# Optimization experiments

Hardware: AMD Instinct MI355X
Metric: run time of the kernel (lower is better)

Reference implementation:

```python
import jax, jax.numpy as jnp
import numpy as np

N = 100000
E = 3200000
NFEAT = 256
NHID = 256
NCLASS = 40


def _uniform(key, shape, stdv):
    return jax.random.uniform(key, shape, jnp.float32, -stdv, stdv)


def setup_inputs() -> dict:
    key = jax.random.key(0)
    ks = jax.random.split(key, 16)
    x = jax.random.normal(ks[0], (N, NFEAT), jnp.float32)
    edge_row = jax.random.randint(ks[1], (E,), 0, N, jnp.int32)
    edge_col = jax.random.randint(ks[2], (E,), 0, N, jnp.int32)
    edge_weight = jax.random.uniform(ks[3], (E,), jnp.float32)
    # MyLinear init: stdv = 1/sqrt(out_features)
    dims = [(NFEAT, NHID), (NHID, NHID), (NHID, NHID), (NHID, NCLASS)]
    params = {}
    for i, (fi, fo) in enumerate(dims):
        stdv = 1.0 / np.sqrt(fo)
        params[f"W{i+1}"] = _uniform(ks[4 + 2 * i], (fi, fo), stdv)
        params[f"b{i+1}"] = _uniform(ks[5 + 2 * i], (fo,), stdv)
    return dict(x=x, edge_row=edge_row, edge_col=edge_col, edge_weight=edge_weight, **params)


def _spmm(edge_row, edge_col, edge_weight, x):
    # out[i] = sum_{(i,j) in E} w_ij * x[j]
    msgs = edge_weight[:, None] * x[edge_col]  # [E, d]
    return jax.ops.segment_sum(msgs, edge_row, num_segments=N)


def reference(x, edge_row, edge_col, edge_weight, W1, b1, W2, b2, W3, b3, W4, b4):
    # layer 0 (ix % mlp_layers == 0 -> residual + spmm)
    h = x + _spmm(edge_row, edge_col, edge_weight, x)
    h = jax.nn.relu(h @ W1 + b1)
    # layer 1
    h = jax.nn.relu(h @ W2 + b2)
    # layer 2 (spmm + residual again)
    h = h + _spmm(edge_row, edge_col, edge_weight, h)
    h = jax.nn.relu(h @ W3 + b3)
    # layer 3 (final, no relu)
    h = h @ W4 + b4
    return jax.nn.log_softmax(h, axis=1)
```

## Files before the change

kernel.cpp:

```cpp
#include <hip/hip_runtime.h>
#include <hip/hip_bf16.h>
#include <cstdint>

#define N_NODES 100000
#define N_EDGES 3200000
#define NFEAT   256
#define NCLASS  40

#define BROWS_LOG 7
#define BROWS     128
#define NBUCK     782
#define CHUNK     8192
#define NBLK      391
#define GHN       (NBUCK * NBLK)

typedef __bf16 bf16;
typedef __attribute__((ext_vector_type(8))) __bf16 bf16x8;
typedef __attribute__((ext_vector_type(4))) float f32x4;
typedef __attribute__((ext_vector_type(2))) float f32x2;

__device__ inline float b2f(unsigned short u) {
    union { unsigned int i; float f; } x; x.i = ((unsigned int)u) << 16; return x.f;
}
__device__ inline unsigned short f2b(float f) {
    union { float f; unsigned int i; } x; x.f = f;
    unsigned int i = x.i;
    return (unsigned short)((i + 0x7fffu + ((i >> 16) & 1u)) >> 16);
}
__device__ inline f32x2 unpack2(unsigned int d) {
    union { unsigned int i; float f; } lo, hi;
    lo.i = d << 16;
    hi.i = d & 0xFFFF0000u;
    return (f32x2){lo.f, hi.f};
}
__device__ inline unsigned int pack2(f32x2 a) {
    return ((unsigned int)f2b(a[0])) | (((unsigned int)f2b(a[1])) << 16);
}

__host__ __device__ inline int permN(int s) {
    return (((s >> 5) & 7) << 5) | (((s >> 2) & 3) << 3) | (((s >> 4) & 1) << 2) | (s & 3);
}

__global__ void prep_w_kernel(const float* __restrict__ W1, const float* __restrict__ W2,
                              const float* __restrict__ W3, const float* __restrict__ W4,
                              const float* __restrict__ b1, const float* __restrict__ b3,
                              unsigned short* __restrict__ WT1, unsigned short* __restrict__ WT2,
                              unsigned short* __restrict__ WT3, unsigned short* __restrict__ WT4,
                              float* __restrict__ b1p, float* __restrict__ b3p) {
    int i = blockIdx.x * blockDim.x + threadIdx.x;
    if (i < 256 * 256) {
        int s = i >> 8, k = i & 255;
        int n = permN(s);
        WT1[i] = f2b(W1[k * 256 + n]);
        WT2[i] = f2b(W2[k * 256 + s]);
        WT3[i] = f2b(W3[k * 256 + n]);
        if (k == 0) { b1p[s] = b1[n]; b3p[s] = b3[n]; }
    }
    if (i < 48 * 256) {
        int nIdx = i >> 8, k = i & 255;
        WT4[i] = (nIdx < NCLASS) ? f2b(W4[k * NCLASS + nIdx]) : (unsigned short)0;
    }
}

__global__ void cast_kernel(const float* __restrict__ X, unsigned short* __restrict__ Y, int n4) {
    int i = blockIdx.x * blockDim.x + threadIdx.x;
    if (i >= n4) return;
    float4 v = *(const float4*)(X + (size_t)i * 4);
    ushort4 o;
    o.x = f2b(v.x); o.y = f2b(v.y); o.z = f2b(v.z); o.w = f2b(v.w);
    *(ushort4*)(Y + (size_t)i * 4) = o;
}

__global__ __launch_bounds__(256) void p1a_kernel(const int* __restrict__ erow,
                                                  int* __restrict__ ghist) {
    __shared__ int h[NBUCK];
    for (int j = threadIdx.x; j < NBUCK; j += 256) h[j] = 0;
    __syncthreads();
    int base = blockIdx.x * CHUNK;
    for (int j = 0; j < CHUNK; j += 256) {
        int i = base + j + threadIdx.x;
        if (i < N_EDGES) atomicAdd(&h[erow[i] >> BROWS_LOG], 1);
    }
    __syncthreads();
    for (int j = threadIdx.x; j < NBUCK; j += 256)
        ghist[(size_t)j * NBLK + blockIdx.x] = h[j];
}

__global__ void scanB_blocks_kernel(int* __restrict__ g, int* __restrict__ bsums, int n) {
    __shared__ int s[1024];
    int i = blockIdx.x * 1024 + threadIdx.x;
    int v = (i < n) ? g[i] : 0;
    s[threadIdx.x] = v;
    __syncthreads();
    for (int off = 1; off < 1024; off <<= 1) {
        int t = (threadIdx.x >= off) ? s[threadIdx.x - off] : 0;
        __syncthreads();
        s[threadIdx.x] += t;
        __syncthreads();
    }
    if (i < n) g[i] = s[threadIdx.x] - v;
    if (threadIdx.x == 1023) bsums[blockIdx.x] = s[1023];
}

__global__ void scanB_sums_kernel(int* __restrict__ bsums, int nb) {
    __shared__ int s[512];
    int v = (threadIdx.x < nb) ? bsums[threadIdx.x] : 0;
    s[threadIdx.x] = v;
    __syncthreads();
    for (int off = 1; off < 512; off <<= 1) {
        int t = (threadIdx.x >= off) ? s[threadIdx.x - off] : 0;
        __syncthreads();
        s[threadIdx.x] += t;
        __syncthreads();
    }
    if (threadIdx.x < nb) bsums[threadIdx.x] = s[threadIdx.x] - v;
}

__global__ void scanB_add_kernel(int* __restrict__ g, const int* __restrict__ bsums, int n) {
    int i = blockIdx.x * blockDim.x + threadIdx.x;
    if (i < n) g[i] += bsums[i >> 10];
}

__global__ __launch_bounds__(256) void p1c_kernel(const int* __restrict__ erow,
                                                  const int* __restrict__ ecol,
                                                  const float* __restrict__ ew,
                                                  const int* __restrict__ ghist,
                                                  uint2* __restrict__ stage) {
    __shared__ int cur[NBUCK];
    for (int j = threadIdx.x; j < NBUCK; j += 256)
        cur[j] = ghist[(size_t)j * NBLK + blockIdx.x];
    __syncthreads();
    int base = blockIdx.x * CHUNK;
    for (int j = 0; j < CHUNK; j += 1024) {
        int r[4], c[4]; float w[4]; bool m[4];
#pragma unroll
        for (int q = 0; q < 4; q++) {
            int i = base + j + q * 256 + threadIdx.x;
            m[q] = (i < N_EDGES);
            if (m[q]) { r[q] = erow[i]; c[q] = ecol[i]; w[q] = ew[i]; }
        }
#pragma unroll
        for (int q = 0; q < 4; q++) {
            if (m[q]) {
                unsigned int qq = (unsigned int)(w[q] * 32768.f + 0.5f);
                if (qq > 32767u) qq = 32767u;
                int p = atomicAdd(&cur[r[q] >> BROWS_LOG], 1);
                stage[p] = make_uint2((unsigned int)r[q], (((unsigned int)c[q]) << 15) | qq);
            }
        }
    }
}

__global__ __launch_bounds__(256) void p2_kernel(const int* __restrict__ ghist,
                                                 const uint2* __restrict__ stage,
                                                 unsigned int* __restrict__ edges,
                                                 int* __restrict__ rowptr) {
    __shared__ int h[BROWS], sc[BROWS], lcur[BROWS];
    int b = blockIdx.x;
    int lo = ghist[(size_t)b * NBLK];
    int hi = (b + 1 < NBUCK) ? ghist[(size_t)(b + 1) * NBLK] : N_EDGES;
    if (threadIdx.x < BROWS) h[threadIdx.x] = 0;
    __syncthreads();
    for (int i = lo + threadIdx.x; i < hi; i += 256)
        atomicAdd(&h[stage[i].x & (BROWS - 1)], 1);
    __syncthreads();
    if (threadIdx.x < BROWS) sc[threadIdx.x] = h[threadIdx.x];
    __syncthreads();
    for (int off = 1; off < BROWS; off <<= 1) {
        int t = 0;
        if (threadIdx.x < BROWS && threadIdx.x >= off) t = sc[threadIdx.x - off];
        __syncthreads();
        if (threadIdx.x < BROWS) sc[threadIdx.x] += t;
        __syncthreads();
    }
    if (threadIdx.x < BROWS) {
        int ex = sc[threadIdx.x] - h[threadIdx.x];
        int row = b * BROWS + threadIdx.x;
        if (row <= N_NODES) rowptr[row] = lo + ex;
        lcur[threadIdx.x] = lo + ex;
    }
    __syncthreads();
    for (int i = lo + threadIdx.x; i < hi; i += 256) {
        uint2 sd = stage[i];
        int p = atomicAdd(&lcur[sd.x & (BROWS - 1)], 1);
        edges[p] = sd.y;
    }
}

__global__ void spmm_res_kernel(const unsigned short* __restrict__ X, unsigned short* __restrict__ Y,
                                const int* __restrict__ rowptr, const unsigned int* __restrict__ edges,
                                int n) {
    int gtid = blockIdx.x * blockDim.x + threadIdx.x;
    int row = gtid >> 6;
    int lane = gtid & 63;
    if (row >= n) return;
    const int half = lane >> 5;
    const int fb = (lane & 31) * 8;

    f32x2 acc[4];
    {
        uint4 xb = *(const uint4*)(X + (size_t)row * NFEAT + fb);
        if (half == 0) {
            acc[0] = unpack2(xb.x); acc[1] = unpack2(xb.y);
            acc[2] = unpack2(xb.z); acc[3] = unpack2(xb.w);
        } else {
            acc[0] = (f32x2){0.f, 0.f}; acc[1] = (f32x2){0.f, 0.f};
            acc[2] = (f32x2){0.f, 0.f}; acc[3] = (f32x2){0.f, 0.f};
        }
    }

    int s = rowptr[row], e = rowptr[row + 1];
    for (int k = s; k < e; k += 12) {
        int   c[6];
        f32x2 w2[6];
#pragma unroll
        for (int j = 0; j < 6; j++) {
            int kj = k + j * 2 + half;
            int kc = (kj < e) ? kj : (e - 1);
            unsigned int d = edges[kc];
            c[j] = (int)(d >> 15);
            float w = (kj < e) ? (float)(d & 32767u) * (1.f / 32768.f) : 0.f;
            w2[j] = (f32x2){w, w};
        }
        uint4 v[6];
#pragma unroll
        for (int j = 0; j < 6; j++) v[j] = *(const uint4*)(X + (size_t)c[j] * NFEAT + fb);
#pragma unroll
        for (int j = 0; j < 6; j++) {
            acc[0] += w2[j] * unpack2(v[j].x);
            acc[1] += w2[j] * unpack2(v[j].y);
            acc[2] += w2[j] * unpack2(v[j].z);
            acc[3] += w2[j] * unpack2(v[j].w);
        }
    }

#pragma unroll
    for (int i = 0; i < 4; i++) {
        acc[i][0] += __shfl_xor(acc[i][0], 32, 64);
        acc[i][1] += __shfl_xor(acc[i][1], 32, 64);
    }
    if (half == 0) {
        uint4 o;
        o.x = pack2(acc[0]); o.y = pack2(acc[1]);
        o.z = pack2(acc[2]); o.w = pack2(acc[3]);
        *(uint4*)(Y + (size_t)row * NFEAT + fb) = o;
    }
}

__global__ __launch_bounds__(256, 4) void gemm12_kernel(
    const bf16* __restrict__ X,
    const bf16* __restrict__ WT1p, const float* __restrict__ b1p,
    const bf16* __restrict__ WT2, const float* __restrict__ b2,
    unsigned short* __restrict__ Y, int M) {
    __shared__ unsigned int sB[256 * 20];
    const int tid = threadIdx.x;
    const int wave = tid >> 6;
    const int lane = tid & 63;
    const int m = lane & 15;
    const int quad = lane >> 4;
    const int lrow = wave * 16 + m;
    const int rowBase = blockIdx.x * 64;
    int arow = rowBase + lrow;
    if (arow >= M) arow = M - 1;

    f32x4 acc[16];
#pragma unroll
    for (int t = 0; t < 16; t++) acc[t] = (f32x4){0.f, 0.f, 0.f, 0.f};

    const bf16* xp = X + (size_t)arow * NFEAT + quad * 8;
#pragma unroll
    for (int k0 = 0; k0 < NFEAT; k0 += 32) {
#pragma unroll
        for (int f = tid; f < 1024; f += 256) {
            int n = f >> 2, j = f & 3;
            uint4 v = *(const uint4*)((const unsigned short*)WT1p + (size_t)n * NFEAT + k0 + j * 8);
            *(uint4*)&sB[n * 20 + j * 4] = v;
        }
        __syncthreads();
        bf16x8 a = *(const bf16x8*)(xp + k0);
#pragma unroll
        for (int t = 0; t < 16; t++) {
            bf16x8 b = *(const bf16x8*)&sB[(t * 16 + m) * 20 + quad * 4];
            acc[t] = __builtin_amdgcn_mfma_f32_16x16x32_bf16(b, a, acc[t], 0, 0, 0);
        }
        __syncthreads();
    }

    bf16x8 af[8];
#pragma unroll
    for (int kc = 0; kc < 8; kc++) {
        const float* p0 = b1p + (2 * kc) * 16 + quad * 4;
        const float* p1 = b1p + (2 * kc + 1) * 16 + quad * 4;
        union { unsigned int u[4]; bf16x8 h; } cv;
        cv.u[0] = pack2((f32x2){fmaxf(acc[2 * kc][0] + p0[0], 0.f),
                                fmaxf(acc[2 * kc][1] + p0[1], 0.f)});
        cv.u[1] = pack2((f32x2){fmaxf(acc[2 * kc][2] + p0[2], 0.f),
                                fmaxf(acc[2 * kc][3] + p0[3], 0.f)});
        cv.u[2] = pack2((f32x2){fmaxf(acc[2 * kc + 1][0] + p1[0], 0.f),
                                fmaxf(acc[2 * kc + 1][1] + p1[1], 0.f)});
        cv.u[3] = pack2((f32x2){fmaxf(acc[2 * kc + 1][2] + p1[2], 0.f),
                                fmaxf(acc[2 * kc + 1][3] + p1[3], 0.f)});
        af[kc] = cv.h;
        acc[2 * kc] = (f32x4){0.f, 0.f, 0.f, 0.f};
        acc[2 * kc + 1] = (f32x4){0.f, 0.f, 0.f, 0.f};
    }

#pragma unroll
    for (int k0 = 0; k0 < NFEAT; k0 += 32) {
#pragma unroll
        for (int f = tid; f < 1024; f += 256) {
            int n = f >> 2, j = f & 3;
            uint4 v = *(const uint4*)((const unsigned short*)WT2 + (size_t)n * NFEAT + k0 + j * 8);
            *(uint4*)&sB[n * 20 + j * 4] = v;
        }
        __syncthreads();
        bf16x8 a = af[k0 >> 5];
#pragma unroll
        for (int t = 0; t < 16; t++) {
            bf16x8 b = *(const bf16x8*)&sB[(t * 16 + m) * 20 + quad * 4];
            acc[t] = __builtin_amdgcn_mfma_f32_16x16x32_bf16(b, a, acc[t], 0, 0, 0);
        }
        __syncthreads();
    }
    const int row = rowBase + lrow;
    if (row < M) {
#pragma unroll
        for (int t = 0; t < 16; t++) {
            const float* bp = b2 + t * 16 + quad * 4;
            f32x2 lo = (f32x2){fmaxf(acc[t][0] + bp[0], 0.f), fmaxf(acc[t][1] + bp[1], 0.f)};
            f32x2 hi = (f32x2){fmaxf(acc[t][2] + bp[2], 0.f), fmaxf(acc[t][3] + bp[3], 0.f)};
            *(uint2*)(Y + (size_t)row * NFEAT + t * 16 + quad * 4) = make_uint2(pack2(lo), pack2(hi));
        }
    }
}

__global__ __launch_bounds__(256, 4) void gemm34_ls_kernel(
    const bf16* __restrict__ X,
    const bf16* __restrict__ WT3p, const float* __restrict__ b3p,
    const bf16* __restrict__ WT4, const float* __restrict__ b4,
    float* __restrict__ out, int M) {
    __shared__ unsigned int sB[256 * 20];
    const int tid = threadIdx.x;
    const int wave = tid >> 6;
    const int lane = tid & 63;
    const int m = lane & 15;
    const int quad = lane >> 4;
    const int lrow = wave * 16 + m;
    const int rowBase = blockIdx.x * 64;
    int arow = rowBase + lrow;
    if (arow >= M) arow = M - 1;

    f32x4 acc[16];
#pragma unroll
    for (int t = 0; t < 16; t++) acc[t] = (f32x4){0.f, 0.f, 0.f, 0.f};

    const bf16* xp = X + (size_t)arow * NFEAT + quad * 8;
#pragma unroll
    for (int k0 = 0; k0 < NFEAT; k0 += 32) {
#pragma unroll
        for (int f = tid; f < 1024; f += 256) {
            int n = f >> 2, j = f & 3;
            uint4 v = *(const uint4*)((const unsigned short*)WT3p + (size_t)n * NFEAT + k0 + j * 8);
            *(uint4*)&sB[n * 20 + j * 4] = v;
        }
        __syncthreads();
        bf16x8 a = *(const bf16x8*)(xp + k0);
#pragma unroll
        for (int t = 0; t < 16; t++) {
            bf16x8 b = *(const bf16x8*)&sB[(t * 16 + m) * 20 + quad * 4];
            acc[t] = __builtin_amdgcn_mfma_f32_16x16x32_bf16(b, a, acc[t], 0, 0, 0);
        }
        __syncthreads();
    }

    bf16x8 af[8];
#pragma unroll
    for (int kc = 0; kc < 8; kc++) {
        const float* p0 = b3p + (2 * kc) * 16 + quad * 4;
        const float* p1 = b3p + (2 * kc + 1) * 16 + quad * 4;
        union { unsigned int u[4]; bf16x8 h; } cv;
        cv.u[0] = pack2((f32x2){fmaxf(acc[2 * kc][0] + p0[0], 0.f),
                                fmaxf(acc[2 * kc][1] + p0[1], 0.f)});
        cv.u[1] = pack2((f32x2){fmaxf(acc[2 * kc][2] + p0[2], 0.f),
                                fmaxf(acc[2 * kc][3] + p0[3], 0.f)});
        cv.u[2] = pack2((f32x2){fmaxf(acc[2 * kc + 1][0] + p1[0], 0.f),
                                fmaxf(acc[2 * kc + 1][1] + p1[1], 0.f)});
        cv.u[3] = pack2((f32x2){fmaxf(acc[2 * kc + 1][2] + p1[2], 0.f),
                                fmaxf(acc[2 * kc + 1][3] + p1[3], 0.f)});
        af[kc] = cv.h;
    }

    f32x4 a4[3];
#pragma unroll
    for (int t = 0; t < 3; t++) a4[t] = (f32x4){0.f, 0.f, 0.f, 0.f};
#pragma unroll
    for (int k0 = 0; k0 < NFEAT; k0 += 32) {
        if (tid < 192) {
            int n = tid >> 2, j = tid & 3;
            uint4 v = *(const uint4*)((const unsigned short*)WT4 + (size_t)n * NFEAT + k0 + j * 8);
            *(uint4*)&sB[n * 20 + j * 4] = v;
        }
        __syncthreads();
        bf16x8 a = af[k0 >> 5];
#pragma unroll
        for (int t = 0; t < 3; t++) {
            bf16x8 b = *(const bf16x8*)&sB[(t * 16 + m) * 20 + quad * 4];
            a4[t] = __builtin_amdgcn_mfma_f32_16x16x32_bf16(b, a, a4[t], 0, 0, 0);
        }
        __syncthreads();
    }

    float v[3][4];
#pragma unroll
    for (int t = 0; t < 3; t++) {
        bool tv = (t < 2) || (quad < 2);
#pragma unroll
        for (int r = 0; r < 4; r++) {
            float bv = tv ? b4[t * 16 + quad * 4 + r] : 0.f;
            v[t][r] = tv ? (a4[t][r] + bv) : -1e30f;
        }
    }

    float mx = -1e30f;
#pragma unroll
    for (int t = 0; t < 3; t++)
#pragma unroll
        for (int r = 0; r < 4; r++) mx = fmaxf(mx, v[t][r]);
    mx = fmaxf(mx, __shfl_xor(mx, 16, 64));
    mx = fmaxf(mx, __shfl_xor(mx, 32, 64));

    float sm = 0.f;
#pragma unroll
    for (int t = 0; t < 3; t++) {
        bool tv = (t < 2) || (quad < 2);
        if (tv) {
#pragma unroll
            for (int r = 0; r < 4; r++) sm += __expf(v[t][r] - mx);
        }
    }
    sm += __shfl_xor(sm, 16, 64);
    sm += __shfl_xor(sm, 32, 64);
    float ls = __logf(sm);

    const int row = rowBase + lrow;
    if (row < M) {
#pragma unroll
        for (int t = 0; t < 3; t++) {
            if ((t < 2) || (quad < 2)) {
                f32x4 o = (f32x4){v[t][0] - mx - ls, v[t][1] - mx - ls,
                                  v[t][2] - mx - ls, v[t][3] - mx - ls};
                *(f32x4*)(out + (size_t)row * NCLASS + t * 16 + quad * 4) = o;
            }
        }
    }
}

extern "C" void kernel_launch(void* const* d_in, const int* in_sizes, int n_in,
                              void* d_out, int out_size, void* d_ws, size_t ws_size,
                              hipStream_t stream) {
    const float* x   = (const float*)d_in[0];
    const int* erow  = (const int*)d_in[1];
    const int* ecol  = (const int*)d_in[2];
    const float* ew  = (const float*)d_in[3];
    const float* W1  = (const float*)d_in[4];
    const float* W2  = (const float*)d_in[6];
    const float* W3  = (const float*)d_in[8];
    const float* W4  = (const float*)d_in[10];
    const float* b1  = (const float*)d_in[5];
    const float* b2  = (const float*)d_in[7];
    const float* b3  = (const float*)d_in[9];
    const float* b4  = (const float*)d_in[11];

    char* ws = (char*)d_ws;
    size_t off = 0;
    auto alloc = [&](size_t bytes) -> char* {
        char* p = ws + off;
        off = (off + bytes + 255) & ~(size_t)255;
        return p;
    };
    int* rowptr  = (int*)alloc((size_t)(N_NODES + 1) * 4);
    int* bsumsB  = (int*)alloc(512 * 4);
    unsigned int* edges = (unsigned int*)alloc((size_t)N_EDGES * 4);
    int* ghist   = (int*)alloc((size_t)GHN * 4);
    unsigned short* WT1 = (unsigned short*)alloc(256 * 256 * 2);
    unsigned short* WT2 = (unsigned short*)alloc(256 * 256 * 2);
    unsigned short* WT3 = (unsigned short*)alloc(256 * 256 * 2);
    unsigned short* WT4 = (unsigned short*)alloc(48 * 256 * 2);
    float* b1p          = (float*)alloc(256 * 4);
    float* b3p          = (float*)alloc(256 * 4);
    unsigned short* hA  = (unsigned short*)alloc((size_t)N_NODES * NFEAT * 2);
    uint2* stage        = (uint2*)hA;
    unsigned short* hB  = (unsigned short*)d_in[0];
    (void)ws_size; (void)n_in; (void)in_sizes; (void)out_size;

    prep_w_kernel<<<(256 * 256 + 255) / 256, 256, 0, stream>>>(
        W1, W2, W3, W4, b1, b3, WT1, WT2, WT3, WT4, b1p, b3p);
    p1a_kernel<<<NBLK, 256, 0, stream>>>(erow, ghist);
    int nsb = (GHN + 1023) / 1024;
    scanB_blocks_kernel<<<nsb, 1024, 0, stream>>>(ghist, bsumsB, GHN);
    scanB_sums_kernel<<<1, 512, 0, stream>>>(bsumsB, nsb);
    scanB_add_kernel<<<(GHN + 255) / 256, 256, 0, stream>>>(ghist, bsumsB, GHN);
    p1c_kernel<<<NBLK, 256, 0, stream>>>(erow, ecol, ew, ghist, stage);
    p2_kernel<<<NBUCK, 256, 0, stream>>>(ghist, stage, edges, rowptr);

    const int n4 = N_NODES * NFEAT / 4;
    const int spmm_grid = (N_NODES * 64 + 255) / 256;
    const int gemm_grid = (N_NODES + 63) / 64;

    cast_kernel<<<(n4 + 255) / 256, 256, 0, stream>>>(x, hA, n4);
    spmm_res_kernel<<<spmm_grid, 256, 0, stream>>>(hA, hB, rowptr, edges, N_NODES);
    gemm12_kernel<<<gemm_grid, 256, 0, stream>>>(
        (const bf16*)hB, (const bf16*)WT1, b1p, (const bf16*)WT2, b2, hB, N_NODES);
    spmm_res_kernel<<<spmm_grid, 256, 0, stream>>>(hB, hA, rowptr, edges, N_NODES);
    gemm34_ls_kernel<<<gemm_grid, 256, 0, stream>>>(
        (const bf16*)hA, (const bf16*)WT3, b3p, (const bf16*)WT4, b4, (float*)d_out, N_NODES);
}
```

Before: 928.6 us.

## Double-buffer GEMM weight tiles, enlarge CSR build chunks, stage p2 scatter in LDS

The two fused GEMM kernels now double-buffer the weight tile in shared memory, prefetching the next K-slice into registers while MFMAs run on the current one. The A row is preloaded into registers, and the second GEMM's first tile is prefetched during the first GEMM's last step. The CSR build uses fewer, larger 512-thread blocks, which shrinks the global histogram and its scan. p2 scatters into an LDS buffer before a coalesced write-out. In exchange, occupancy drops from 4 to 3 blocks per SM and shared memory use per block grows.

```diff
diff --git a/kernel.cpp b/kernel.cpp
--- a/kernel.cpp
+++ b/kernel.cpp
@@ -10,9 +10,10 @@
 #define BROWS_LOG 7
 #define BROWS     128
 #define NBUCK     782
-#define CHUNK     8192
-#define NBLK      391
+#define CHUNK     32768
+#define NBLK      98
 #define GHN       (NBUCK * NBLK)
+#define P2CAP     8192
 
 typedef __bf16 bf16;
 typedef __attribute__((ext_vector_type(8))) __bf16 bf16x8;
@@ -71,18 +72,18 @@
     *(ushort4*)(Y + (size_t)i * 4) = o;
 }
 
-__global__ __launch_bounds__(256) void p1a_kernel(const int* __restrict__ erow,
+__global__ __launch_bounds__(512) void p1a_kernel(const int* __restrict__ erow,
                                                   int* __restrict__ ghist) {
     __shared__ int h[NBUCK];
-    for (int j = threadIdx.x; j < NBUCK; j += 256) h[j] = 0;
+    for (int j = threadIdx.x; j < NBUCK; j += 512) h[j] = 0;
     __syncthreads();
     int base = blockIdx.x * CHUNK;
-    for (int j = 0; j < CHUNK; j += 256) {
+    for (int j = 0; j < CHUNK; j += 512) {
         int i = base + j + threadIdx.x;
         if (i < N_EDGES) atomicAdd(&h[erow[i] >> BROWS_LOG], 1);
     }
     __syncthreads();
-    for (int j = threadIdx.x; j < NBUCK; j += 256)
+    for (int j = threadIdx.x; j < NBUCK; j += 512)
         ghist[(size_t)j * NBLK + blockIdx.x] = h[j];
 }
 
@@ -121,21 +122,21 @@
     if (i < n) g[i] += bsums[i >> 10];
 }
 
-__global__ __launch_bounds__(256) void p1c_kernel(const int* __restrict__ erow,
+__global__ __launch_bounds__(512) void p1c_kernel(const int* __restrict__ erow,
                                                   const int* __restrict__ ecol,
                                                   const float* __restrict__ ew,
                                                   const int* __restrict__ ghist,
                                                   uint2* __restrict__ stage) {
     __shared__ int cur[NBUCK];
-    for (int j = threadIdx.x; j < NBUCK; j += 256)
+    for (int j = threadIdx.x; j < NBUCK; j += 512)
         cur[j] = ghist[(size_t)j * NBLK + blockIdx.x];
     __syncthreads();
     int base = blockIdx.x * CHUNK;
-    for (int j = 0; j < CHUNK; j += 1024) {
+    for (int j = 0; j < CHUNK; j += 2048) {
         int r[4], c[4]; float w[4]; bool m[4];
 #pragma unroll
         for (int q = 0; q < 4; q++) {
-            int i = base + j + q * 256 + threadIdx.x;
+            int i = base + j + q * 512 + threadIdx.x;
             m[q] = (i < N_EDGES);
             if (m[q]) { r[q] = erow[i]; c[q] = ecol[i]; w[q] = ew[i]; }
         }
@@ -156,9 +157,11 @@
                                                  unsigned int* __restrict__ edges,
                                                  int* __restrict__ rowptr) {
     __shared__ int h[BROWS], sc[BROWS], lcur[BROWS];
+    __shared__ unsigned int buf[P2CAP];
     int b = blockIdx.x;
     int lo = ghist[(size_t)b * NBLK];
     int hi = (b + 1 < NBUCK) ? ghist[(size_t)(b + 1) * NBLK] : N_EDGES;
+    int cnt = hi - lo;
     if (threadIdx.x < BROWS) h[threadIdx.x] = 0;
     __syncthreads();
     for (int i = lo + threadIdx.x; i < hi; i += 256)
@@ -177,13 +180,24 @@
         int ex = sc[threadIdx.x] - h[threadIdx.x];
         int row = b * BROWS + threadIdx.x;
         if (row <= N_NODES) rowptr[row] = lo + ex;
-        lcur[threadIdx.x] = lo + ex;
-    }
-    __syncthreads();
-    for (int i = lo + threadIdx.x; i < hi; i += 256) {
-        uint2 sd = stage[i];
-        int p = atomicAdd(&lcur[sd.x & (BROWS - 1)], 1);
-        edges[p] = sd.y;
+        lcur[threadIdx.x] = (cnt <= P2CAP) ? ex : (lo + ex);
+    }
+    __syncthreads();
+    if (cnt <= P2CAP) {
+        for (int i = lo + threadIdx.x; i < hi; i += 256) {
+            uint2 sd = stage[i];
+            int p = atomicAdd(&lcur[sd.x & (BROWS - 1)], 1);
+            buf[p] = sd.y;
+        }
+        __syncthreads();
+        for (int i = threadIdx.x; i < cnt; i += 256)
+            edges[lo + i] = buf[i];
+    } else {
+        for (int i = lo + threadIdx.x; i < hi; i += 256) {
+            uint2 sd = stage[i];
+            int p = atomicAdd(&lcur[sd.x & (BROWS - 1)], 1);
+            edges[p] = sd.y;
+        }
     }
 }
 
@@ -247,12 +261,31 @@
     }
 }
 
-__global__ __launch_bounds__(256, 4) void gemm12_kernel(
+template <int NT>
+__device__ __forceinline__ void stage_issue(const unsigned short* __restrict__ WT, int k0,
+                                            uint4 (&st)[4], int tid) {
+#pragma unroll
+    for (int f = tid, i = 0; f < NT * 64; f += 256, ++i) {
+        int n = f >> 2, j = f & 3;
+        st[i] = *(const uint4*)(WT + (size_t)n * NFEAT + k0 + j * 8);
+    }
+}
+template <int NT>
+__device__ __forceinline__ void stage_write(unsigned int* __restrict__ sB,
+                                            const uint4 (&st)[4], int tid) {
+#pragma unroll
+    for (int f = tid, i = 0; f < NT * 64; f += 256, ++i) {
+        int n = f >> 2, j = f & 3;
+        *(uint4*)&sB[n * 20 + j * 4] = st[i];
+    }
+}
+
+__global__ __launch_bounds__(256, 3) void gemm12_kernel(
     const bf16* __restrict__ X,
     const bf16* __restrict__ WT1p, const float* __restrict__ b1p,
     const bf16* __restrict__ WT2, const float* __restrict__ b2,
     unsigned short* __restrict__ Y, int M) {
-    __shared__ unsigned int sB[256 * 20];
+    __shared__ unsigned int sB[2][256 * 20];
     const int tid = threadIdx.x;
     const int wave = tid >> 6;
     const int lane = tid & 63;
@@ -263,26 +296,34 @@
     int arow = rowBase + lrow;
     if (arow >= M) arow = M - 1;
 
+    const bf16* xp = X + (size_t)arow * NFEAT + quad * 8;
+    bf16x8 a[8];
+#pragma unroll
+    for (int kk = 0; kk < 8; ++kk) a[kk] = *(const bf16x8*)(xp + kk * 32);
+
     f32x4 acc[16];
 #pragma unroll
     for (int t = 0; t < 16; t++) acc[t] = (f32x4){0.f, 0.f, 0.f, 0.f};
 
-    const bf16* xp = X + (size_t)arow * NFEAT + quad * 8;
-#pragma unroll
-    for (int k0 = 0; k0 < NFEAT; k0 += 32) {
-#pragma unroll
-        for (int f = tid; f < 1024; f += 256) {
-            int n = f >> 2, j = f & 3;
-            uint4 v = *(const uint4*)((const unsigned short*)WT1p + (size_t)n * NFEAT + k0 + j * 8);
-            *(uint4*)&sB[n * 20 + j * 4] = v;
-        }
-        __syncthreads();
-        bf16x8 a = *(const bf16x8*)(xp + k0);
+    uint4 st[4];
+    stage_issue<16>((const unsigned short*)WT1p, 0, st, tid);
+    stage_write<16>(sB[0], st, tid);
+    __syncthreads();
+
+#pragma unroll
+    for (int k = 0; k < 8; ++k) {
+        unsigned int* curB = sB[k & 1];
+        unsigned int* nxtB = sB[(k + 1) & 1];
+        const unsigned short* nsrc = (k < 7) ? (const unsigned short*)WT1p
+                                             : (const unsigned short*)WT2;
+        stage_issue<16>(nsrc, (k < 7) ? (k + 1) * 32 : 0, st, tid);
+        bf16x8 av = a[k];
 #pragma unroll
         for (int t = 0; t < 16; t++) {
-            bf16x8 b = *(const bf16x8*)&sB[(t * 16 + m) * 20 + quad * 4];
-            acc[t] = __builtin_amdgcn_mfma_f32_16x16x32_bf16(b, a, acc[t], 0, 0, 0);
-        }
+            bf16x8 b = *(const bf16x8*)&curB[(t * 16 + m) * 20 + quad * 4];
+            acc[t] = __builtin_amdgcn_mfma_f32_16x16x32_bf16(b, av, acc[t], 0, 0, 0);
+        }
+        stage_write<16>(nxtB, st, tid);
         __syncthreads();
     }
 
@@ -306,22 +347,22 @@
     }
 
 #pragma unroll
-    for (int k0 = 0; k0 < NFEAT; k0 += 32) {
-#pragma unroll
-        for (int f = tid; f < 1024; f += 256) {
-            int n = f >> 2, j = f & 3;
-            uint4 v = *(const uint4*)((const unsigned short*)WT2 + (size_t)n * NFEAT + k0 + j * 8);
-            *(uint4*)&sB[n * 20 + j * 4] = v;
-        }
-        __syncthreads();
-        bf16x8 a = af[k0 >> 5];
+    for (int k = 0; k < 8; ++k) {
+        unsigned int* curB = sB[k & 1];
+        unsigned int* nxtB = sB[(k + 1) & 1];
+        if (k < 7) stage_issue<16>((const unsigned short*)WT2, (k + 1) * 32, st, tid);
+        bf16x8 av = af[k];
 #pragma unroll
         for (int t = 0; t < 16; t++) {
-            bf16x8 b = *(const bf16x8*)&sB[(t * 16 + m) * 20 + quad * 4];
-            acc[t] = __builtin_amdgcn_mfma_f32_16x16x32_bf16(b, a, acc[t], 0, 0, 0);
-        }
-        __syncthreads();
-    }
+            bf16x8 b = *(const bf16x8*)&curB[(t * 16 + m) * 20 + quad * 4];
+            acc[t] = __builtin_amdgcn_mfma_f32_16x16x32_bf16(b, av, acc[t], 0, 0, 0);
+        }
+        if (k < 7) {
+            stage_write<16>(nxtB, st, tid);
+            __syncthreads();
+        }
+    }
+
     const int row = rowBase + lrow;
     if (row < M) {
 #pragma unroll
@@ -334,12 +375,12 @@
     }
 }
 
-__global__ __launch_bounds__(256, 4) void gemm34_ls_kernel(
+__global__ __launch_bounds__(256, 3) void gemm34_ls_kernel(
     const bf16* __restrict__ X,
     const bf16* __restrict__ WT3p, const float* __restrict__ b3p,
     const bf16* __restrict__ WT4, const float* __restrict__ b4,
     float* __restrict__ out, int M) {
-    __shared__ unsigned int sB[256 * 20];
+    __shared__ unsigned int sB[2][256 * 20];
     const int tid = threadIdx.x;
     const int wave = tid >> 6;
     const int lane = tid & 63;
@@ -350,26 +391,34 @@
     int arow = rowBase + lrow;
     if (arow >= M) arow = M - 1;
 
+    const bf16* xp = X + (size_t)arow * NFEAT + quad * 8;
+    bf16x8 a[8];
+#pragma unroll
+    for (int kk = 0; kk < 8; ++kk) a[kk] = *(const bf16x8*)(xp + kk * 32);
+
     f32x4 acc[16];
 #pragma unroll
     for (int t = 0; t < 16; t++) acc[t] = (f32x4){0.f, 0.f, 0.f, 0.f};
 
-    const bf16* xp = X + (size_t)arow * NFEAT + quad * 8;
-#pragma unroll
-    for (int k0 = 0; k0 < NFEAT; k0 += 32) {
-#pragma unroll
-        for (int f = tid; f < 1024; f += 256) {
-            int n = f >> 2, j = f & 3;
-            uint4 v = *(const uint4*)((const unsigned short*)WT3p + (size_t)n * NFEAT + k0 + j * 8);
-            *(uint4*)&sB[n * 20 + j * 4] = v;
-        }
-        __syncthreads();
-        bf16x8 a = *(const bf16x8*)(xp + k0);
+    uint4 st[4];
+    stage_issue<16>((const unsigned short*)WT3p, 0, st, tid);
+    stage_write<16>(sB[0], st, tid);
+    __syncthreads();
+
+#pragma unroll
+    for (int k = 0; k < 8; ++k) {
+        unsigned int* curB = sB[k & 1];
+        unsigned int* nxtB = sB[(k + 1) & 1];
+        if (k < 7) stage_issue<16>((const unsigned short*)WT3p, (k + 1) * 32, st, tid);
+        else       stage_issue<3>((const unsigned short*)WT4, 0, st, tid);
+        bf16x8 av = a[k];
 #pragma unroll
         for (int t = 0; t < 16; t++) {
-            bf16x8 b = *(const bf16x8*)&sB[(t * 16 + m) * 20 + quad * 4];
-            acc[t] = __builtin_amdgcn_mfma_f32_16x16x32_bf16(b, a, acc[t], 0, 0, 0);
-        }
+            bf16x8 b = *(const bf16x8*)&curB[(t * 16 + m) * 20 + quad * 4];
+            acc[t] = __builtin_amdgcn_mfma_f32_16x16x32_bf16(b, av, acc[t], 0, 0, 0);
+        }
+        if (k < 7) stage_write<16>(nxtB, st, tid);
+        else       stage_write<3>(nxtB, st, tid);
         __syncthreads();
     }
 
@@ -394,20 +443,20 @@
 #pragma unroll
     for (int t = 0; t < 3; t++) a4[t] = (f32x4){0.f, 0.f, 0.f, 0.f};
 #pragma unroll
-    for (int k0 = 0; k0 < NFEAT; k0 += 32) {
-        if (tid < 192) {
-            int n = tid >> 2, j = tid & 3;
-            uint4 v = *(const uint4*)((const unsigned short*)WT4 + (size_t)n * NFEAT + k0 + j * 8);
-            *(uint4*)&sB[n * 20 + j * 4] = v;
-        }
-        __syncthreads();
-        bf16x8 a = af[k0 >> 5];
+    for (int k = 0; k < 8; ++k) {
+        unsigned int* curB = sB[k & 1];
+        unsigned int* nxtB = sB[(k + 1) & 1];
+        if (k < 7) stage_issue<3>((const unsigned short*)WT4, (k + 1) * 32, st, tid);
+        bf16x8 av = af[k];
 #pragma unroll
         for (int t = 0; t < 3; t++) {
-            bf16x8 b = *(const bf16x8*)&sB[(t * 16 + m) * 20 + quad * 4];
-            a4[t] = __builtin_amdgcn_mfma_f32_16x16x32_bf16(b, a, a4[t], 0, 0, 0);
-        }
-        __syncthreads();
+            bf16x8 b = *(const bf16x8*)&curB[(t * 16 + m) * 20 + quad * 4];
+            a4[t] = __builtin_amdgcn_mfma_f32_16x16x32_bf16(b, av, a4[t], 0, 0, 0);
+        }
+        if (k < 7) {
+            stage_write<3>(nxtB, st, tid);
+            __syncthreads();
+        }
     }
 
     float v[3][4];
@@ -495,12 +544,12 @@
 
     prep_w_kernel<<<(256 * 256 + 255) / 256, 256, 0, stream>>>(
         W1, W2, W3, W4, b1, b3, WT1, WT2, WT3, WT4, b1p, b3p);
-    p1a_kernel<<<NBLK, 256, 0, stream>>>(erow, ghist);
+    p1a_kernel<<<NBLK, 512, 0, stream>>>(erow, ghist);
     int nsb = (GHN + 1023) / 1024;
     scanB_blocks_kernel<<<nsb, 1024, 0, stream>>>(ghist, bsumsB, GHN);
     scanB_sums_kernel<<<1, 512, 0, stream>>>(bsumsB, nsb);
     scanB_add_kernel<<<(GHN + 255) / 256, 256, 0, stream>>>(ghist, bsumsB, GHN);
-    p1c_kernel<<<NBLK, 256, 0, stream>>>(erow, ecol, ew, ghist, stage);
+    p1c_kernel<<<NBLK, 512, 0, stream>>>(erow, ecol, ew, ghist, stage);
     p2_kernel<<<NBUCK, 256, 0, stream>>>(ghist, stage, edges, rowptr);
 
     const int n4 = N_NODES * NFEAT / 4;
```

New measurement: 1.034 ms. 11.4% more time.
